# Kernel optimization log

Measured on AMD Instinct MI355X. Metric: run time of the kernel, lower is better.

Reference implementation:

```python
import jax, jax.numpy as jnp
import numpy as np

N_NODES = 50000
N_EDGES = 800000
F_IN = 128
EMB = 256
N_GRAPHS = 512


def _linear_params(key, fan_out, fan_in, dtype=jnp.float32):
    kw, kb = jax.random.split(key)
    scale = 1.0 / np.sqrt(fan_in)
    W = jax.random.normal(kw, (fan_out, fan_in), dtype) * scale
    b = jnp.zeros((fan_out,), dtype)
    return W, b


def setup_inputs() -> dict:
    key = jax.random.key(0)
    ks = jax.random.split(key, 8)
    x = jax.random.normal(ks[0], (N_NODES, F_IN), jnp.float32)
    edge_index = jax.random.randint(ks[1], (2, N_EDGES), 0, N_NODES, dtype=jnp.int64)
    batch_index = jnp.sort(jax.random.randint(ks[2], (N_NODES,), 0, N_GRAPHS, dtype=jnp.int64))
    W0, b0 = _linear_params(ks[3], EMB, F_IN)            # initial_conv: 128 -> 256
    W1, b1 = _linear_params(ks[4], EMB // 2, EMB)        # conv1: 256 -> 128
    W2, b2 = _linear_params(ks[5], EMB // 4, EMB // 2)   # conv2: 128 -> 64
    W3, b3 = _linear_params(ks[6], EMB // 8, EMB // 4)   # conv3: 64 -> 32
    Wout, bout = _linear_params(ks[7], 1, EMB // 4)      # out: 64 -> 1 (gmp||gap of 32)
    return {"x": x, "edge_index": edge_index, "batch_index": batch_index,
            "num_graphs": N_GRAPHS,
            "W0": W0, "b0": b0, "W1": W1, "b1": b1, "W2": W2, "b2": b2,
            "W3": W3, "b3": b3, "Wout": Wout, "bout": bout}


def _gcn_conv(x, W, b, src, dst, deg_inv_sqrt, n):
    # PyG GCNConv: h = X W^T; out_i = sum_{j->i} norm_ij h_j + (1/deg_i) h_i + b
    h = x @ W.T
    norm = deg_inv_sqrt[src] * deg_inv_sqrt[dst]          # [E]
    agg = jax.ops.segment_sum(h[src] * norm[:, None], dst, num_segments=n)
    agg = agg + h * (deg_inv_sqrt * deg_inv_sqrt)[:, None]  # self-loop term
    return agg + b


def reference(x, edge_index, batch_index, num_graphs, W0, b0, W1, b1, W2, b2, W3, b3, Wout, bout):
    n = x.shape[0]
    src, dst = edge_index[0], edge_index[1]
    # symmetric GCN normalization with self-loops: deg = in-degree + 1
    deg = jax.ops.segment_sum(jnp.ones(src.shape[0], x.dtype), dst, num_segments=n) + 1.0
    dis = jax.lax.rsqrt(deg)
    h = jnp.tanh(_gcn_conv(x, W0, b0, src, dst, dis, n))
    h = jnp.tanh(_gcn_conv(h, W1, b1, src, dst, dis, n))
    h = jnp.tanh(_gcn_conv(h, W2, b2, src, dst, dis, n))
    h = jnp.tanh(_gcn_conv(h, W3, b3, src, dst, dis, n))   # [N, 32]
    counts = jax.ops.segment_sum(jnp.ones(n, h.dtype), batch_index, num_segments=num_graphs)
    maxp = jax.ops.segment_max(h, batch_index, num_segments=num_graphs)
    maxp = jnp.where(counts[:, None] > 0, maxp, 0.0)
    meanp = jax.ops.segment_sum(h, batch_index, num_segments=num_graphs) / jnp.maximum(counts, 1.0)[:, None]
    pooled = jnp.concatenate([maxp, meanp], axis=1)        # [G, 64]
    return pooled @ Wout.T + bout                          # [G, 1]
```

## Files before the change

### kernel.cpp

```cpp
#include <hip/hip_runtime.h>
#include <hip/hip_bf16.h>
#include <math.h>


#define THREADS 256

typedef __attribute__((ext_vector_type(8))) short bf16x8;
typedef __attribute__((ext_vector_type(4))) float f32x4;

__device__ inline unsigned short f2bf(float f) {
    unsigned int u = __float_as_uint(f);
    u += 0x7FFFu + ((u >> 16) & 1u);
    return (unsigned short)(u >> 16);
}

__device__ inline void cvt8(uint4 v, float* f) {
    f[0] = __uint_as_float(v.x << 16); f[1] = __uint_as_float(v.x & 0xFFFF0000u);
    f[2] = __uint_as_float(v.y << 16); f[3] = __uint_as_float(v.y & 0xFFFF0000u);
    f[4] = __uint_as_float(v.z << 16); f[5] = __uint_as_float(v.z & 0xFFFF0000u);
    f[6] = __uint_as_float(v.w << 16); f[7] = __uint_as_float(v.w & 0xFFFF0000u);
}

__global__ void f32_to_bf16(const float* __restrict__ in,
                            unsigned short* __restrict__ out, int n4) {
    for (int i = blockIdx.x * blockDim.x + threadIdx.x; i < n4;
         i += gridDim.x * blockDim.x) {
        float4 v = ((const float4*)in)[i];
        ushort4 h;
        h.x = f2bf(v.x); h.y = f2bf(v.y); h.z = f2bf(v.z); h.w = f2bf(v.w);
        ((ushort4*)out)[i] = h;
    }
}


__global__ void count_dst(const int* __restrict__ dst, int E, int* __restrict__ cnt) {
    int e = blockIdx.x * blockDim.x + threadIdx.x;
    if (e < E) atomicAdd(&cnt[dst[e]], 1);
}

__global__ void compute_dis(const int* __restrict__ cnt, float* __restrict__ dis, int N) {
    int i = blockIdx.x * blockDim.x + threadIdx.x;
    if (i < N) dis[i] = rsqrtf((float)cnt[i] + 1.0f);
}

__global__ void scan_phase1(const int* __restrict__ cnt, int N, int* __restrict__ bsums) {
    __shared__ int s[256];
    int i = blockIdx.x * 256 + threadIdx.x;
    int v = (i < N) ? cnt[i] : 0;
    s[threadIdx.x] = v; __syncthreads();
    for (int off = 128; off > 0; off >>= 1) {
        if (threadIdx.x < off) s[threadIdx.x] += s[threadIdx.x + off];
        __syncthreads();
    }
    if (threadIdx.x == 0) bsums[blockIdx.x] = s[0];
}

__global__ void scan_small_excl(const int* __restrict__ in, int* __restrict__ out,
                                int n, int total) {
    __shared__ int s[1024];
    int t = threadIdx.x;
    int v = (t < n) ? in[t] : 0;
    s[t] = v; __syncthreads();
    for (int off = 1; off < 1024; off <<= 1) {
        int x = (t >= off) ? s[t - off] : 0;
        __syncthreads();
        s[t] += x;
        __syncthreads();
    }
    if (t < n) out[t] = s[t] - v;
    if (t == 0) out[n] = total;
}

__global__ void scan_phase3(const int* __restrict__ cnt, int N,
                            const int* __restrict__ bsums_scanned,
                            int* __restrict__ off, int* __restrict__ cursor, int E) {
    __shared__ int s[256];
    int i = blockIdx.x * 256 + threadIdx.x;
    int v = (i < N) ? cnt[i] : 0;
    s[threadIdx.x] = v; __syncthreads();
    for (int o = 1; o < 256; o <<= 1) {
        int x = (threadIdx.x >= o) ? s[threadIdx.x - o] : 0;
        __syncthreads();
        s[threadIdx.x] += x;
        __syncthreads();
    }
    if (i < N) {
        int val = bsums_scanned[blockIdx.x] + s[threadIdx.x] - v;
        off[i] = val;
        cursor[i] = val;
    }
    if (blockIdx.x == 0 && threadIdx.x == 0) off[N] = E;
}

__global__ void fill_csr(const int* __restrict__ src, const int* __restrict__ dst, int E,
                         int* __restrict__ cursor, int* __restrict__ csr_src) {
    int e = blockIdx.x * blockDim.x + threadIdx.x;
    if (e < E) {
        int p = atomicAdd(&cursor[dst[e]], 1);
        csr_src[p] = src[e];
    }
}

__global__ void count_batch(const int* __restrict__ batch, int N, int* __restrict__ gcnt) {
    int i = blockIdx.x * blockDim.x + threadIdx.x;
    if (i < N) atomicAdd(&gcnt[batch[i]], 1);
}

template<int F, bool FUSE, bool OUT16>
__global__ void aggregate_bf16(const unsigned short* __restrict__ t,
                               const int* __restrict__ off,
                               const int* __restrict__ csr_src,
                               const float* __restrict__ dis,
                               const float* __restrict__ bias,
                               void* __restrict__ outv, int N) {
    constexpr int TPN = F / 8, NPB = THREADS / TPN;
    int node = blockIdx.x * NPB + threadIdx.x / TPN;
    int lane = threadIdx.x % TPN;
    if (node >= N) return;
    const uint4* tp = (const uint4*)t;
    float di = dis[node];
    int s0 = off[node], s1 = off[node + 1];

    float acc[8], f[8];
    cvt8(tp[(size_t)node * TPN + lane], f);
#pragma unroll
    for (int j = 0; j < 8; ++j) acc[j] = di * di * f[j];

    int k = s0;
    for (; k + 7 < s1; k += 8) {
        int i0 = csr_src[k + 0], i1 = csr_src[k + 1];
        int i2 = csr_src[k + 2], i3 = csr_src[k + 3];
        int i4 = csr_src[k + 4], i5 = csr_src[k + 5];
        int i6 = csr_src[k + 6], i7 = csr_src[k + 7];
        float n0 = di * dis[i0], n1 = di * dis[i1];
        float n2 = di * dis[i2], n3 = di * dis[i3];
        float n4 = di * dis[i4], n5 = di * dis[i5];
        float n6 = di * dis[i6], n7 = di * dis[i7];
        uint4 v0 = tp[(size_t)i0 * TPN + lane];
        uint4 v1 = tp[(size_t)i1 * TPN + lane];
        uint4 v2 = tp[(size_t)i2 * TPN + lane];
        uint4 v3 = tp[(size_t)i3 * TPN + lane];
        uint4 v4 = tp[(size_t)i4 * TPN + lane];
        uint4 v5 = tp[(size_t)i5 * TPN + lane];
        uint4 v6 = tp[(size_t)i6 * TPN + lane];
        uint4 v7 = tp[(size_t)i7 * TPN + lane];
        cvt8(v0, f);
#pragma unroll
        for (int j = 0; j < 8; ++j) acc[j] += n0 * f[j];
        cvt8(v1, f);
#pragma unroll
        for (int j = 0; j < 8; ++j) acc[j] += n1 * f[j];
        cvt8(v2, f);
#pragma unroll
        for (int j = 0; j < 8; ++j) acc[j] += n2 * f[j];
        cvt8(v3, f);
#pragma unroll
        for (int j = 0; j < 8; ++j) acc[j] += n3 * f[j];
        cvt8(v4, f);
#pragma unroll
        for (int j = 0; j < 8; ++j) acc[j] += n4 * f[j];
        cvt8(v5, f);
#pragma unroll
        for (int j = 0; j < 8; ++j) acc[j] += n5 * f[j];
        cvt8(v6, f);
#pragma unroll
        for (int j = 0; j < 8; ++j) acc[j] += n6 * f[j];
        cvt8(v7, f);
#pragma unroll
        for (int j = 0; j < 8; ++j) acc[j] += n7 * f[j];
    }
    for (; k < s1; ++k) {
        int s = csr_src[k];
        float nr = di * dis[s];
        cvt8(tp[(size_t)s * TPN + lane], f);
#pragma unroll
        for (int j = 0; j < 8; ++j) acc[j] += nr * f[j];
    }
    if (FUSE) {
        float4 b0 = ((const float4*)bias)[lane * 2 + 0];
        float4 b1 = ((const float4*)bias)[lane * 2 + 1];
        acc[0] = tanhf(acc[0] + b0.x); acc[1] = tanhf(acc[1] + b0.y);
        acc[2] = tanhf(acc[2] + b0.z); acc[3] = tanhf(acc[3] + b0.w);
        acc[4] = tanhf(acc[4] + b1.x); acc[5] = tanhf(acc[5] + b1.y);
        acc[6] = tanhf(acc[6] + b1.z); acc[7] = tanhf(acc[7] + b1.w);
    }
    if constexpr (OUT16) {
        uint4 o;
        o.x = (unsigned)f2bf(acc[0]) | ((unsigned)f2bf(acc[1]) << 16);
        o.y = (unsigned)f2bf(acc[2]) | ((unsigned)f2bf(acc[3]) << 16);
        o.z = (unsigned)f2bf(acc[4]) | ((unsigned)f2bf(acc[5]) << 16);
        o.w = (unsigned)f2bf(acc[6]) | ((unsigned)f2bf(acc[7]) << 16);
        ((uint4*)outv)[(size_t)node * TPN + lane] = o;
    } else {
        float* op = (float*)outv + (size_t)node * F + lane * 8;
        float4 o0 = {acc[0], acc[1], acc[2], acc[3]};
        float4 o1 = {acc[4], acc[5], acc[6], acc[7]};
        *(float4*)op = o0;
        *(float4*)(op + 4) = o1;
    }
}

template<int K, int FOUT, int BN, bool ACT, bool OUT16>
__global__ __launch_bounds__(256) void gemm_mfma(const unsigned short* __restrict__ A,
                                                 const float* __restrict__ W,
                                                 const float* __restrict__ bias,
                                                 void* __restrict__ Cv, int N) {
    constexpr int BM = 64, BK = 32;
    constexpr int MF = 2;
    constexpr int NF = BN / 32;
    constexpr int LR = 40;
    __shared__ unsigned short Al[BM * LR];
    __shared__ unsigned short Bl[BN * LR];
    const int tid = threadIdx.x;
    const int bm = blockIdx.x * BM, bn = blockIdx.y * BN;
    const int wv = tid >> 6, ln = tid & 63;
    const int fro = (wv >> 1) * 32, fco = (wv & 1) * (BN / 2);
    const int l15 = ln & 15, lc = ln >> 4;
    f32x4 zero = {0.f, 0.f, 0.f, 0.f};
    f32x4 acc[MF][NF];
#pragma unroll
    for (int i = 0; i < MF; ++i)
#pragma unroll
        for (int j = 0; j < NF; ++j) acc[i][j] = zero;

    for (int k0 = 0; k0 < K; k0 += BK) {
        for (int u = tid; u < BM * 4; u += 256) {
            int r = u >> 2, q = u & 3;
            int row = bm + r;
            uint4 v = make_uint4(0, 0, 0, 0);
            if (row < N) v = *(const uint4*)&A[(size_t)row * K + k0 + q * 8];
            *(uint4*)&Al[r * LR + q * 8] = v;
        }
        for (int u = tid; u < BN * 8; u += 256) {
            int r = u >> 3, q = u & 7;
            float4 v = *(const float4*)&W[(size_t)(bn + r) * K + k0 + q * 4];
            ushort4 h;
            h.x = f2bf(v.x); h.y = f2bf(v.y); h.z = f2bf(v.z); h.w = f2bf(v.w);
            *(ushort4*)&Bl[r * LR + q * 4] = h;
        }
        __syncthreads();
        bf16x8 a[MF], b[NF];
#pragma unroll
        for (int f = 0; f < MF; ++f)
            a[f] = *(const bf16x8*)&Al[(fro + f * 16 + l15) * LR + lc * 8];
#pragma unroll
        for (int f = 0; f < NF; ++f)
            b[f] = *(const bf16x8*)&Bl[(fco + f * 16 + l15) * LR + lc * 8];
#pragma unroll
        for (int i = 0; i < MF; ++i)
#pragma unroll
            for (int j = 0; j < NF; ++j)
                acc[i][j] = __builtin_amdgcn_mfma_f32_16x16x32_bf16(a[i], b[j], acc[i][j], 0, 0, 0);
        __syncthreads();
    }
#pragma unroll
    for (int i = 0; i < MF; ++i) {
#pragma unroll
        for (int j = 0; j < NF; ++j) {
            int col = bn + fco + j * 16 + l15;
#pragma unroll
            for (int rg = 0; rg < 4; ++rg) {
                int row = bm + fro + i * 16 + lc * 4 + rg;
                if (row < N) {
                    float v = acc[i][j][rg];
                    if (ACT) v = tanhf(v + bias[col]);
                    if constexpr (OUT16)
                        ((unsigned short*)Cv)[(size_t)row * FOUT + col] = f2bf(v);
                    else
                        ((float*)Cv)[(size_t)row * FOUT + col] = v;
                }
            }
        }
    }
}

__global__ void pool_out(const float* __restrict__ h, const int* __restrict__ goff,
                         const float* __restrict__ Wout, const float* __restrict__ bout,
                         float* __restrict__ out) {
    int g = blockIdx.x;
    int s0 = goff[g], s1 = goff[g + 1];
    int f = threadIdx.x % 32;
    int sl = threadIdx.x / 32;
    float mx = -INFINITY, sm = 0.f;
    for (int i = s0 + sl; i < s1; i += 8) {
        float v = h[(size_t)i * 32 + f];
        mx = fmaxf(mx, v);
        sm += v;
    }
    __shared__ float smx[256], ssm[256];
    smx[threadIdx.x] = mx; ssm[threadIdx.x] = sm; __syncthreads();
    for (int off = 128; off >= 32; off >>= 1) {
        if (threadIdx.x < off) {
            smx[threadIdx.x] = fmaxf(smx[threadIdx.x], smx[threadIdx.x + off]);
            ssm[threadIdx.x] += ssm[threadIdx.x + off];
        }
        __syncthreads();
    }
    int cnt = s1 - s0;
    if (threadIdx.x < 32) {
        float maxp = (cnt > 0) ? smx[threadIdx.x] : 0.f;
        float meanp = ssm[threadIdx.x] / fmaxf((float)cnt, 1.f);
        float part = maxp * Wout[threadIdx.x] + meanp * Wout[32 + threadIdx.x];
        for (int o = 16; o > 0; o >>= 1) part += __shfl_down(part, o);
        if (threadIdx.x == 0) out[g] = part + bout[0];
    }
}


extern "C" void kernel_launch(void* const* d_in, const int* in_sizes, int n_in,
                              void* d_out, int out_size, void* d_ws, size_t ws_size,
                              hipStream_t stream) {
    const float* x      = (const float*)d_in[0];
    const int*   ei     = (const int*)d_in[1];
    const int*   batch  = (const int*)d_in[2];
    const float* W0 = (const float*)d_in[4];
    const float* b0 = (const float*)d_in[5];
    const float* W1 = (const float*)d_in[6];
    const float* b1 = (const float*)d_in[7];
    const float* W2 = (const float*)d_in[8];
    const float* b2 = (const float*)d_in[9];
    const float* W3 = (const float*)d_in[10];
    const float* b3 = (const float*)d_in[11];
    const float* Wout = (const float*)d_in[12];
    const float* bout = (const float*)d_in[13];
    float* out = (float*)d_out;

    const int N = in_sizes[0] / 128;
    const int E = in_sizes[1] / 2;
    const int G = out_size;
    const int* src = ei;
    const int* dst = ei + E;

    char* p = (char*)d_ws;
    auto alloc = [&](size_t bytes) {
        char* r = p;
        p += (bytes + 255) & ~(size_t)255;
        return r;
    };
    int*   cnt     = (int*)alloc((size_t)N * 4);
    int*   cursor  = (int*)alloc((size_t)N * 4);
    int*   csr_off = (int*)alloc((size_t)(N + 1) * 4);
    float* dis     = (float*)alloc((size_t)N * 4);
    int*   bsums   = (int*)alloc(1024 * 4);
    int*   gcnt    = (int*)alloc((size_t)G * 4);
    int*   goff    = (int*)alloc((size_t)(G + 1) * 4);
    int*   csr_src = (int*)alloc((size_t)E * 4);
    float* bufA    = (float*)alloc((size_t)N * 256 * 4);
    float* bufB    = (float*)alloc((size_t)N * 128 * 4);
    float* bufC    = (float*)alloc((size_t)N * 128 * 4);
    unsigned short* x16 = (unsigned short*)alloc((size_t)N * 128 * 2);
    unsigned short* bufA16 = (unsigned short*)bufA;
    unsigned short* bufB16 = (unsigned short*)bufB;
    unsigned short* bufC16 = (unsigned short*)bufC;

    hipMemsetAsync(cnt, 0, (size_t)N * 4, stream);
    hipMemsetAsync(gcnt, 0, (size_t)G * 4, stream);

    int ebl = (E + THREADS - 1) / THREADS;
    int nbl = (N + THREADS - 1) / THREADS;
    int B   = (N + 255) / 256;

    f32_to_bf16<<<2048, THREADS, 0, stream>>>(x, x16, N * 128 / 4);
    count_dst<<<ebl, THREADS, 0, stream>>>(dst, E, cnt);
    compute_dis<<<nbl, THREADS, 0, stream>>>(cnt, dis, N);
    scan_phase1<<<B, 256, 0, stream>>>(cnt, N, bsums);
    scan_small_excl<<<1, 1024, 0, stream>>>(bsums, bsums, B, E);
    scan_phase3<<<B, 256, 0, stream>>>(cnt, N, bsums, csr_off, cursor, E);
    fill_csr<<<ebl, THREADS, 0, stream>>>(src, dst, E, cursor, csr_src);
    count_batch<<<nbl, THREADS, 0, stream>>>(batch, N, gcnt);
    scan_small_excl<<<1, 1024, 0, stream>>>(gcnt, goff, G, N);

    aggregate_bf16<128, false, true><<<(N + 15) / 16, THREADS, 0, stream>>>(
        x16, csr_off, csr_src, dis, nullptr, bufB16, N);
    {
        dim3 grid((N + 63) / 64, 4);
        gemm_mfma<128, 256, 64, true, true><<<grid, 256, 0, stream>>>(bufB16, W0, b0, bufA16, N);
    }
    {
        dim3 grid((N + 63) / 64, 2);
        gemm_mfma<256, 128, 64, false, true><<<grid, 256, 0, stream>>>(bufA16, W1, nullptr, bufC16, N);
    }
    aggregate_bf16<128, true, true><<<(N + 15) / 16, THREADS, 0, stream>>>(
        bufC16, csr_off, csr_src, dis, b1, bufB16, N);
    {
        dim3 grid((N + 63) / 64, 1);
        gemm_mfma<128, 64, 64, false, true><<<grid, 256, 0, stream>>>(bufB16, W2, nullptr, bufC16, N);
    }
    aggregate_bf16<64, true, true><<<(N + 31) / 32, THREADS, 0, stream>>>(
        bufC16, csr_off, csr_src, dis, b2, bufA16, N);
    {
        dim3 grid((N + 63) / 64, 1);
        gemm_mfma<64, 32, 32, false, true><<<grid, 256, 0, stream>>>(bufA16, W3, nullptr, bufC16, N);
    }
    aggregate_bf16<32, true, false><<<(N + 63) / 64, THREADS, 0, stream>>>(
        bufC16, csr_off, csr_src, dis, b3, bufB, N);

    pool_out<<<G, 256, 0, stream>>>(bufB, goff, Wout, bout, out);
}
```

Measured before the change: 335.7 us.

## Fuse preprocessing kernels and split CSR fill into destination-range passes

Merges the bf16 conversion of x, the destination-degree count and the graph-size count into one grid-stride prologue kernel. It also folds the rsqrt degree normalisation into the first scan phase. Together these remove several small launches and extra passes over memory. The CSR fill is now split into eight launches, each handling a slice of destination nodes, to keep atomic cursor updates and scattered csr_src writes within a smaller, cache-resident region. The cost is reading the full edge list eight times plus seven extra launches, and the fused prologue relies on the conversion loop count covering both E and N.

```diff
diff --git a/kernel.cpp b/kernel.cpp
--- a/kernel.cpp
+++ b/kernel.cpp
@@ -21,32 +21,28 @@
     f[6] = __uint_as_float(v.w << 16); f[7] = __uint_as_float(v.w & 0xFFFF0000u);
 }
 
-__global__ void f32_to_bf16(const float* __restrict__ in,
-                            unsigned short* __restrict__ out, int n4) {
-    for (int i = blockIdx.x * blockDim.x + threadIdx.x; i < n4;
-         i += gridDim.x * blockDim.x) {
-        float4 v = ((const float4*)in)[i];
+__global__ void prologue(const float* __restrict__ x, unsigned short* __restrict__ x16,
+                         int n4, const int* __restrict__ dst, int E,
+                         int* __restrict__ cnt, const int* __restrict__ batch,
+                         int N, int* __restrict__ gcnt) {
+    int stride = gridDim.x * blockDim.x;
+    for (int i = blockIdx.x * blockDim.x + threadIdx.x; i < n4; i += stride) {
+        float4 v = ((const float4*)x)[i];
         ushort4 h;
         h.x = f2bf(v.x); h.y = f2bf(v.y); h.z = f2bf(v.z); h.w = f2bf(v.w);
-        ((ushort4*)out)[i] = h;
-    }
-}
-
-
-__global__ void count_dst(const int* __restrict__ dst, int E, int* __restrict__ cnt) {
-    int e = blockIdx.x * blockDim.x + threadIdx.x;
-    if (e < E) atomicAdd(&cnt[dst[e]], 1);
-}
-
-__global__ void compute_dis(const int* __restrict__ cnt, float* __restrict__ dis, int N) {
-    int i = blockIdx.x * blockDim.x + threadIdx.x;
-    if (i < N) dis[i] = rsqrtf((float)cnt[i] + 1.0f);
-}
-
-__global__ void scan_phase1(const int* __restrict__ cnt, int N, int* __restrict__ bsums) {
+        ((ushort4*)x16)[i] = h;
+        if (i < E) atomicAdd(&cnt[dst[i]], 1);
+        if (i < N) atomicAdd(&gcnt[batch[i]], 1);
+    }
+}
+
+
+__global__ void scan_phase1(const int* __restrict__ cnt, int N,
+                            int* __restrict__ bsums, float* __restrict__ dis) {
     __shared__ int s[256];
     int i = blockIdx.x * 256 + threadIdx.x;
     int v = (i < N) ? cnt[i] : 0;
+    if (i < N) dis[i] = rsqrtf((float)v + 1.0f);
     s[threadIdx.x] = v; __syncthreads();
     for (int off = 128; off > 0; off >>= 1) {
         if (threadIdx.x < off) s[threadIdx.x] += s[threadIdx.x + off];
@@ -92,18 +88,17 @@
     if (blockIdx.x == 0 && threadIdx.x == 0) off[N] = E;
 }
 
-__global__ void fill_csr(const int* __restrict__ src, const int* __restrict__ dst, int E,
-                         int* __restrict__ cursor, int* __restrict__ csr_src) {
+__global__ void fill_csr_range(const int* __restrict__ src, const int* __restrict__ dst,
+                               int E, int* __restrict__ cursor,
+                               int* __restrict__ csr_src, int lo, int hi) {
     int e = blockIdx.x * blockDim.x + threadIdx.x;
     if (e < E) {
-        int p = atomicAdd(&cursor[dst[e]], 1);
-        csr_src[p] = src[e];
-    }
-}
-
-__global__ void count_batch(const int* __restrict__ batch, int N, int* __restrict__ gcnt) {
-    int i = blockIdx.x * blockDim.x + threadIdx.x;
-    if (i < N) atomicAdd(&gcnt[batch[i]], 1);
+        int d = dst[e];
+        if (d >= lo && d < hi) {
+            int p = atomicAdd(&cursor[d], 1);
+            csr_src[p] = src[e];
+        }
+    }
 }
 
 template<int F, bool FUSE, bool OUT16>
@@ -356,18 +351,23 @@
     hipMemsetAsync(cnt, 0, (size_t)N * 4, stream);
     hipMemsetAsync(gcnt, 0, (size_t)G * 4, stream);
 
-    int ebl = (E + THREADS - 1) / THREADS;
-    int nbl = (N + THREADS - 1) / THREADS;
-    int B   = (N + 255) / 256;
-
-    f32_to_bf16<<<2048, THREADS, 0, stream>>>(x, x16, N * 128 / 4);
-    count_dst<<<ebl, THREADS, 0, stream>>>(dst, E, cnt);
-    compute_dis<<<nbl, THREADS, 0, stream>>>(cnt, dis, N);
-    scan_phase1<<<B, 256, 0, stream>>>(cnt, N, bsums);
+    int B = (N + 255) / 256;
+
+    prologue<<<2048, THREADS, 0, stream>>>(x, x16, N * 128 / 4, dst, E, cnt,
+                                           batch, N, gcnt);
+    scan_phase1<<<B, 256, 0, stream>>>(cnt, N, bsums, dis);
     scan_small_excl<<<1, 1024, 0, stream>>>(bsums, bsums, B, E);
     scan_phase3<<<B, 256, 0, stream>>>(cnt, N, bsums, csr_off, cursor, E);
-    fill_csr<<<ebl, THREADS, 0, stream>>>(src, dst, E, cursor, csr_src);
-    count_batch<<<nbl, THREADS, 0, stream>>>(batch, N, gcnt);
+    {
+        int ebl = (E + THREADS - 1) / THREADS;
+        int chunk = (N + 7) / 8;
+        for (int r = 0; r < 8; ++r) {
+            int lo = r * chunk;
+            int hi = (lo + chunk < N) ? lo + chunk : N;
+            fill_csr_range<<<ebl, THREADS, 0, stream>>>(src, dst, E, cursor,
+                                                        csr_src, lo, hi);
+        }
+    }
     scan_small_excl<<<1, 1024, 0, stream>>>(gcnt, goff, G, N);
 
     aggregate_bf16<128, false, true><<<(N + 15) / 16, THREADS, 0, stream>>>(
```

After: 334.2 us. Within noise of the previous version (-0.4%).
